# Performance work log

Hardware: AMD Instinct MI355X
Metric: run time of the kernel (lower is better)

Reference implementation:

```python
import jax, jax.numpy as jnp
import numpy as np

K = 2048          # codebook / vocab size (HMM N)
T = 1024          # time steps (HMM M)
NNZ = 4096        # sparse likelihood entries per mixture code (padded, static)
B = 16            # beam width
TEMPERATURE = 0.7


def setup_inputs() -> dict:
    key = jax.random.key(0)
    k0, k1, k2, k3, k4, k5 = jax.random.split(key, 6)
    prior0_table = jax.random.normal(k0, (K, K), dtype=jnp.float32)
    prior1_table = jax.random.normal(k1, (K, K), dtype=jnp.float32)
    # sparse log-likelihood values (log-domain, negative-ish)
    ll_data = jax.random.normal(k2, (T, NNZ), dtype=jnp.float32) - 2.0
    # coords: pairs (x0, x1) with nonzero likelihood for each mixture code
    ll_coords = jax.random.randint(k3, (T, 2, NNZ), 0, K, dtype=jnp.int32)
    x0_init = jax.random.randint(k4, (B,), 0, K, dtype=jnp.int32)  # SOS tokens
    x1_init = jax.random.randint(k5, (B,), 0, K, dtype=jnp.int32)
    return {"prior0_table": prior0_table, "prior1_table": prior1_table,
            "ll_data": ll_data, "ll_coords": ll_coords,
            "x0_init": x0_init, "x1_init": x1_init}


def _normalize_logits(logits, temperature):
    return jax.nn.log_softmax(logits / temperature, axis=-1)


def reference(prior0_table, prior1_table, ll_data, ll_coords, x0_init, x1_init):
    def step(carry, inputs):
        x0, x1, log_post_sum = carry            # [B], [B], [B]
        coords, data = inputs                   # [2, NNZ], [NNZ]
        log_p_0 = _normalize_logits(prior0_table[x0], TEMPERATURE)  # [B, K]
        log_p_1 = _normalize_logits(prior1_table[x1], TEMPERATURE)  # [B, K]
        # fused log posterior over sparse likelihood support: [B, NNZ]
        posterior = (log_post_sum[:, None] + data[None, :]
                     + log_p_0[:, coords[0]] + log_p_1[:, coords[1]])
        vals, idx = jax.lax.top_k(posterior.reshape(-1), B)  # prune to B beams
        coords_idx = idx % NNZ
        nx0 = coords[0, coords_idx]
        nx1 = coords[1, coords_idx]
        return (nx0, nx1, vals), (nx0, nx1)

    init = (x0_init, x1_init, jnp.zeros((B,), dtype=jnp.float32))
    (x0, x1, log_post_sum), (seq0, seq1) = jax.lax.scan(
        step, init, (ll_coords, ll_data))
    # final beam scores and decoded token sequences [T, B]
    return log_post_sum, seq0, seq1
```

## Files before the change

### kernel.cpp

```cpp
#include <hip/hip_runtime.h>
#include <hip/hip_bf16.h>
#include <math.h>
#include <stdint.h>

#define KDIM   2048
#define TSTEPS 1024
#define NNZ    4096
#define BEAMS  16
#define NWG    16
#define EPT    16
#define LCAP   4096

__device__ __forceinline__ float post_val(float lpsb, float d,
                                          float v0, float mm0, float ll0,
                                          float v1, float mm1, float ll1) {
    return ((lpsb + d) + ((v0 - mm0) - ll0)) + ((v1 - mm1) - ll1);
}

__device__ __forceinline__ uint32_t ord_enc(float f) {
    uint32_t u = __float_as_uint(f);
    return (u & 0x80000000u) ? ~u : (u | 0x80000000u);
}
__device__ __forceinline__ float ord_dec(uint32_t u) {
    return __uint_as_float((u & 0x80000000u) ? (u & 0x7FFFFFFFu) : ~u);
}

__global__ void scale_kernel(const float* __restrict__ p0,
                             const float* __restrict__ p1,
                             float* __restrict__ sc) {
    const int NF4 = (KDIM * KDIM) / 4;
    int i = blockIdx.x * blockDim.x + threadIdx.x;
    float4 v;
    if (i < NF4) v = ((const float4*)p0)[i];
    else         v = ((const float4*)p1)[i - NF4];
    v.x = v.x / 0.7f; v.y = v.y / 0.7f; v.z = v.z / 0.7f; v.w = v.w / 0.7f;
    ((float4*)sc)[i] = v;
}

__global__ void rowstat_kernel(const float* __restrict__ sc,
                               float* __restrict__ mArr,
                               float* __restrict__ lArr) {
    __shared__ float red[4];
    __shared__ float bm;
    const int r = blockIdx.x;
    const float* row = sc + (size_t)r * KDIM;
    const int tid = threadIdx.x;
    const int lane = tid & 63, wv = tid >> 6;

    float4 a = ((const float4*)row)[tid];
    float4 b = ((const float4*)row)[tid + 256];
    float m = fmaxf(fmaxf(fmaxf(a.x, a.y), fmaxf(a.z, a.w)),
                    fmaxf(fmaxf(b.x, b.y), fmaxf(b.z, b.w)));
    for (int s = 32; s; s >>= 1) m = fmaxf(m, __shfl_xor(m, s));
    if (lane == 0) red[wv] = m;
    __syncthreads();
    if (tid == 0) bm = fmaxf(fmaxf(red[0], red[1]), fmaxf(red[2], red[3]));
    __syncthreads();
    const float mm = bm;

    float s = expf(a.x - mm);
    s += expf(a.y - mm); s += expf(a.z - mm); s += expf(a.w - mm);
    s += expf(b.x - mm); s += expf(b.y - mm); s += expf(b.z - mm); s += expf(b.w - mm);
    for (int sh = 32; sh; sh >>= 1) s += __shfl_xor(s, sh);
    __syncthreads();
    if (lane == 0) red[wv] = s;
    __syncthreads();
    if (tid == 0) {
        float S = ((red[0] + red[1]) + red[2]) + red[3];
        mArr[r] = mm;
        lArr[r] = logf(S);
    }
}

__device__ __forceinline__ void bitonic64(float& v, int& i, int lane) {
    for (int k = 2; k <= 64; k <<= 1) {
        for (int j = k >> 1; j > 0; j >>= 1) {
            float ov = __shfl_xor(v, j);
            int   oi = __shfl_xor(i, j);
            bool lower = (lane & j) == 0;
            bool up    = (lane & k) == 0;
            bool iwin  = (v > ov) || (v == ov && i < oi);
            bool take  = (lower == up) ? !iwin : iwin;
            if (take) { v = ov; i = oi; }
        }
    }
}

__device__ __forceinline__ uint64_t bsort64(uint64_t v, int lane) {
    for (int k = 2; k <= 64; k <<= 1) {
        for (int j = k >> 1; j > 0; j >>= 1) {
            uint64_t ov = __shfl_xor((unsigned long long)v, j);
            bool lower = (lane & j) == 0;
            bool up    = (lane & k) == 0;
            bool iwin  = v > ov;
            bool take  = (lower == up) ? !iwin : iwin;
            if (take) v = ov;
        }
    }
    return v;
}

__device__ __forceinline__ float wave16th(float v, int lane) {
    int i = lane;
    bitonic64(v, i, lane);
    return __shfl(v, 15);
}

__device__ __forceinline__ void wave_top16(int C, float* cv, int* ci, int lane,
                                           float& myv, int& myi) {
    myv = -INFINITY; myi = 0x7FFFFFFF;
    if (C <= 64) {
        float v = (lane < C) ? cv[lane] : -INFINITY;
        int   i = (lane < C) ? ci[lane] : 0x7FFFFFFF;
        bitonic64(v, i, lane);
        myv = v; myi = i;
    } else {
        for (int rk = 0; rk < BEAMS; ++rk) {
            float bv = -INFINITY; int bi = 0x7FFFFFFF, bj = -1;
            for (int j = lane; j < C; j += 64) {
                float v = cv[j]; int ii = ci[j];
                if (v > bv || (v == bv && ii < bi)) { bv = v; bi = ii; bj = j; }
            }
            for (int s = 32; s; s >>= 1) {
                float ov = __shfl_xor(bv, s);
                int   oi = __shfl_xor(bi, s);
                int   oj = __shfl_xor(bj, s);
                if (ov > bv || (ov == bv && oi < bi)) { bv = ov; bi = oi; bj = oj; }
            }
            if (lane == rk) { myv = bv; myi = bi; }
            if (lane == 0) cv[bj] = -INFINITY;
        }
    }
}

__global__ __launch_bounds__(256, 1) void beam_kernel(
    const float* __restrict__ sc,
    const float* __restrict__ mArr,
    const float* __restrict__ lArr,
    const float* __restrict__ ll_data,
    const int*   __restrict__ ll_coords,
    const int*   __restrict__ x0i,
    const int*   __restrict__ x1i,
    float* __restrict__ out,
    uint64_t* __restrict__ gslot)
{
    __shared__ int   sx0[BEAMS], sx1[BEAMS];
    __shared__ float slps[BEAMS];
    __shared__ float wred[4];
    __shared__ int   scnt;
    __shared__ float cand_v[LCAP];
    __shared__ int   cand_i[LCAP];
    __shared__ uint64_t mg[64];
    __shared__ uint64_t respk[BEAMS];

    const int tid  = threadIdx.x;
    const int lane = tid & 63;
    const int wv   = tid >> 6;
    const int b    = blockIdx.x;
    const float* sc1 = sc + (size_t)KDIM * KDIM;
    const int n0 = tid * EPT;

    if (tid < BEAMS) { sx0[tid] = x0i[tid]; sx1[tid] = x1i[tid]; slps[tid] = 0.0f; }
    __syncthreads();

    float4 pf_d[4]; int4 pf_a[4], pf_b[4];
#pragma unroll
    for (int j = 0; j < 4; ++j) {
        pf_d[j] = *(const float4*)(ll_data + n0 + 4 * j);
        pf_a[j] = *(const int4*)(ll_coords + n0 + 4 * j);
        pf_b[j] = *(const int4*)(ll_coords + NNZ + n0 + 4 * j);
    }

#pragma unroll 1
    for (int t = 0; t < TSTEPS; ++t) {
        const int* cp = ll_coords + (size_t)t * 2 * NNZ;
        uint64_t* slots = gslot + (size_t)(t & 1) * (NWG * BEAMS);
        const uint32_t tag = (uint32_t)(t + 1);

        const int   r0i = sx0[b], r1i = sx1[b];
        const float* r0 = sc  + (size_t)r0i * KDIM;
        const float* r1 = sc1 + (size_t)r1i * KDIM;
        const float mm0 = mArr[r0i],        ll0 = lArr[r0i];
        const float mm1 = mArr[KDIM + r1i], ll1 = lArr[KDIM + r1i];
        const float lpsb = slps[b];

        if (tid == 0) scnt = 0;
        float p[EPT];
        float best = -INFINITY;
#pragma unroll
        for (int j = 0; j < 4; ++j) {
            float4 d4 = pf_d[j]; int4 a4 = pf_a[j]; int4 b4 = pf_b[j];
            float va0 = r0[a4.x], va1 = r0[a4.y], va2 = r0[a4.z], va3 = r0[a4.w];
            float vb0 = r1[b4.x], vb1 = r1[b4.y], vb2 = r1[b4.z], vb3 = r1[b4.w];
            p[4*j+0] = post_val(lpsb, d4.x, va0, mm0, ll0, vb0, mm1, ll1);
            p[4*j+1] = post_val(lpsb, d4.y, va1, mm0, ll0, vb1, mm1, ll1);
            p[4*j+2] = post_val(lpsb, d4.z, va2, mm0, ll0, vb2, mm1, ll1);
            p[4*j+3] = post_val(lpsb, d4.w, va3, mm0, ll0, vb3, mm1, ll1);
            best = fmaxf(best, fmaxf(fmaxf(p[4*j+0], p[4*j+1]), fmaxf(p[4*j+2], p[4*j+3])));
        }

        float w16 = wave16th(best, lane);
        if (lane == 0) wred[wv] = w16;
        __syncthreads();
        const float tau = fmaxf(fmaxf(wred[0], wred[1]), fmaxf(wred[2], wred[3]));

        if (best >= tau) {
#pragma unroll
            for (int j = 0; j < EPT; ++j) {
                if (p[j] >= tau) {
                    int pos = atomicAdd(&scnt, 1);
                    cand_v[pos] = p[j]; cand_i[pos] = (b << 12) | (n0 + j);
                }
            }
        }
        __syncthreads();

        {
            const int tp = (t + 1 < TSTEPS) ? t + 1 : t;
            const float* dp2 = ll_data + (size_t)tp * NNZ;
            const int*   cp2 = ll_coords + (size_t)tp * 2 * NNZ;
#pragma unroll
            for (int j = 0; j < 4; ++j) {
                pf_d[j] = *(const float4*)(dp2 + n0 + 4 * j);
                pf_a[j] = *(const int4*)(cp2 + n0 + 4 * j);
                pf_b[j] = *(const int4*)(cp2 + NNZ + n0 + 4 * j);
            }
        }

        if (wv == 0) {
            float myv; int myi;
            wave_top16(scnt, cand_v, cand_i, lane, myv, myi);
            if (lane < BEAMS) {
                uint64_t pk = ((uint64_t)ord_enc(myv) << 32)
                            | ((uint64_t)tag << 16)
                            | (uint64_t)((myi ^ 0xFFFF) & 0xFFFF);
                __hip_atomic_store(&slots[b * BEAMS + lane], pk,
                                   __ATOMIC_RELAXED, __HIP_MEMORY_SCOPE_AGENT);
            }
        }

        uint64_t pk;
        do {
            pk = __hip_atomic_load(&slots[tid], __ATOMIC_RELAXED,
                                   __HIP_MEMORY_SCOPE_AGENT);
        } while (((uint32_t)(pk >> 16) & 0xFFFFu) != tag);

        pk = bsort64(pk, lane);
        if (lane < BEAMS) mg[wv * BEAMS + lane] = pk;
        __syncthreads();
        if (wv == 0) {
            uint64_t q = bsort64(mg[lane], lane);
            if (lane < BEAMS) respk[lane] = q;
        }
        __syncthreads();

        if (tid < BEAMS) {
            uint64_t q = respk[tid];
            float v = ord_dec((uint32_t)(q >> 32));
            int idx = (int)((q & 0xFFFFu) ^ 0xFFFFu);
            int n = idx & (NNZ - 1);
            int tok0 = cp[n];
            int tok1 = cp[NNZ + n];
            sx0[tid] = tok0; sx1[tid] = tok1; slps[tid] = v;
            if (b == 0) {
                out[BEAMS + (size_t)t * BEAMS + tid] = (float)tok0;
                out[BEAMS + (size_t)TSTEPS * BEAMS + (size_t)t * BEAMS + tid] = (float)tok1;
                if (t == TSTEPS - 1) out[tid] = v;
            }
        }
        __syncthreads();
    }
}

extern "C" void kernel_launch(void* const* d_in, const int* in_sizes, int n_in,
                              void* d_out, int out_size, void* d_ws, size_t ws_size,
                              hipStream_t stream) {
    const float* p0        = (const float*)d_in[0];
    const float* p1        = (const float*)d_in[1];
    const float* ll_data   = (const float*)d_in[2];
    const int*   ll_coords = (const int*)d_in[3];
    const int*   x0i       = (const int*)d_in[4];
    const int*   x1i       = (const int*)d_in[5];
    float* outp = (float*)d_out;

    float* sc   = (float*)d_ws;
    float* mArr = sc + (size_t)2 * KDIM * KDIM;
    float* lArr = mArr + 2 * KDIM;
    uint64_t* gslot = (uint64_t*)(lArr + 2 * KDIM);

    scale_kernel<<<(2 * KDIM * KDIM / 4) / 256, 256, 0, stream>>>(p0, p1, sc);
    rowstat_kernel<<<2 * KDIM, 256, 0, stream>>>(sc, mArr, lArr);
    beam_kernel<<<NWG, 256, 0, stream>>>(sc, mArr, lArr, ll_data, ll_coords,
                                         x0i, x1i, outp, gslot);
}
```

Baseline: 17.71 ms.

## Pack candidates as u64 keys, ballot-compact them, and threshold-prune the cross-workgroup merge

Candidates are now stored as packed 64-bit (ordered value, index) keys, so selection compares one integer instead of value plus index. They are appended to LDS through wave ballot plus mbcnt, which replaces one LDS atomic per element with one per wave. The global merge takes the minimum of each workgroup's head key as a threshold and keeps only keys at or above it before a single wave selects the top 16. That replaces the two-level bitonic merge and lets every thread read its next beam state from registers. Spin polling now sleeps between tries, and the linear top-16 fallback on large candidate sets may cost more per step.

```diff
diff --git a/kernel.cpp b/kernel.cpp
--- a/kernel.cpp
+++ b/kernel.cpp
@@ -23,6 +23,11 @@
 }
 __device__ __forceinline__ float ord_dec(uint32_t u) {
     return __uint_as_float((u & 0x80000000u) ? (u & 0x7FFFFFFFu) : ~u);
+}
+
+__device__ __forceinline__ int lane_offset(uint64_t mask) {
+    return __builtin_amdgcn_mbcnt_hi((uint32_t)(mask >> 32),
+           __builtin_amdgcn_mbcnt_lo((uint32_t)mask, 0u));
 }
 
 __global__ void scale_kernel(const float* __restrict__ p0,
@@ -72,18 +77,18 @@
     }
 }
 
-__device__ __forceinline__ void bitonic64(float& v, int& i, int lane) {
+__device__ __forceinline__ float wave16th_f(float v, int lane) {
     for (int k = 2; k <= 64; k <<= 1) {
         for (int j = k >> 1; j > 0; j >>= 1) {
             float ov = __shfl_xor(v, j);
-            int   oi = __shfl_xor(i, j);
             bool lower = (lane & j) == 0;
             bool up    = (lane & k) == 0;
-            bool iwin  = (v > ov) || (v == ov && i < oi);
+            bool iwin  = v > ov;
             bool take  = (lower == up) ? !iwin : iwin;
-            if (take) { v = ov; i = oi; }
-        }
-    }
+            if (take) v = ov;
+        }
+    }
+    return __shfl(v, 15);
 }
 
 __device__ __forceinline__ uint64_t bsort64(uint64_t v, int lane) {
@@ -100,37 +105,27 @@
     return v;
 }
 
-__device__ __forceinline__ float wave16th(float v, int lane) {
-    int i = lane;
-    bitonic64(v, i, lane);
-    return __shfl(v, 15);
-}
-
-__device__ __forceinline__ void wave_top16(int C, float* cv, int* ci, int lane,
-                                           float& myv, int& myi) {
-    myv = -INFINITY; myi = 0x7FFFFFFF;
+__device__ __forceinline__ uint64_t wave_sel16_u64(int C, uint64_t* lds, int lane) {
     if (C <= 64) {
-        float v = (lane < C) ? cv[lane] : -INFINITY;
-        int   i = (lane < C) ? ci[lane] : 0x7FFFFFFF;
-        bitonic64(v, i, lane);
-        myv = v; myi = i;
-    } else {
-        for (int rk = 0; rk < BEAMS; ++rk) {
-            float bv = -INFINITY; int bi = 0x7FFFFFFF, bj = -1;
-            for (int j = lane; j < C; j += 64) {
-                float v = cv[j]; int ii = ci[j];
-                if (v > bv || (v == bv && ii < bi)) { bv = v; bi = ii; bj = j; }
-            }
-            for (int s = 32; s; s >>= 1) {
-                float ov = __shfl_xor(bv, s);
-                int   oi = __shfl_xor(bi, s);
-                int   oj = __shfl_xor(bj, s);
-                if (ov > bv || (ov == bv && oi < bi)) { bv = ov; bi = oi; bj = oj; }
-            }
-            if (lane == rk) { myv = bv; myi = bi; }
-            if (lane == 0) cv[bj] = -INFINITY;
-        }
-    }
+        uint64_t v = (lane < C) ? lds[lane] : 0;
+        return bsort64(v, lane);
+    }
+    uint64_t res = 0;
+    for (int rk = 0; rk < BEAMS; ++rk) {
+        uint64_t bv = 0; int bj = -1;
+        for (int j = lane; j < C; j += 64) {
+            uint64_t v = lds[j];
+            if (v > bv) { bv = v; bj = j; }
+        }
+        for (int s = 32; s; s >>= 1) {
+            uint64_t ov = __shfl_xor((unsigned long long)bv, s);
+            int      oj = __shfl_xor(bj, s);
+            if (ov > bv) { bv = ov; bj = oj; }
+        }
+        if (lane == 0 && bj >= 0) lds[bj] = 0;
+        if (lane == rk) res = bv;
+    }
+    return res;
 }
 
 __global__ __launch_bounds__(256, 1) void beam_kernel(
@@ -144,13 +139,10 @@
     float* __restrict__ out,
     uint64_t* __restrict__ gslot)
 {
-    __shared__ int   sx0[BEAMS], sx1[BEAMS];
-    __shared__ float slps[BEAMS];
-    __shared__ float wred[4];
-    __shared__ int   scnt;
-    __shared__ float cand_v[LCAP];
-    __shared__ int   cand_i[LCAP];
-    __shared__ uint64_t mg[64];
+    __shared__ float    wred[4];
+    __shared__ int      scnt;
+    __shared__ uint64_t cand_pk[LCAP];
+    __shared__ uint64_t headq[NWG];
     __shared__ uint64_t respk[BEAMS];
 
     const int tid  = threadIdx.x;
@@ -160,8 +152,9 @@
     const float* sc1 = sc + (size_t)KDIM * KDIM;
     const int n0 = tid * EPT;
 
-    if (tid < BEAMS) { sx0[tid] = x0i[tid]; sx1[tid] = x1i[tid]; slps[tid] = 0.0f; }
-    __syncthreads();
+    int   r0i  = x0i[b];
+    int   r1i  = x1i[b];
+    float lpsb = 0.0f;
 
     float4 pf_d[4]; int4 pf_a[4], pf_b[4];
 #pragma unroll
@@ -177,14 +170,13 @@
         uint64_t* slots = gslot + (size_t)(t & 1) * (NWG * BEAMS);
         const uint32_t tag = (uint32_t)(t + 1);
 
-        const int   r0i = sx0[b], r1i = sx1[b];
+        if (tid == 0) scnt = 0;
+
         const float* r0 = sc  + (size_t)r0i * KDIM;
         const float* r1 = sc1 + (size_t)r1i * KDIM;
         const float mm0 = mArr[r0i],        ll0 = lArr[r0i];
         const float mm1 = mArr[KDIM + r1i], ll1 = lArr[KDIM + r1i];
-        const float lpsb = slps[b];
-
-        if (tid == 0) scnt = 0;
+
         float p[EPT];
         float best = -INFINITY;
 #pragma unroll
@@ -199,21 +191,10 @@
             best = fmaxf(best, fmaxf(fmaxf(p[4*j+0], p[4*j+1]), fmaxf(p[4*j+2], p[4*j+3])));
         }
 
-        float w16 = wave16th(best, lane);
+        float w16 = wave16th_f(best, lane);
         if (lane == 0) wred[wv] = w16;
         __syncthreads();
         const float tau = fmaxf(fmaxf(wred[0], wred[1]), fmaxf(wred[2], wred[3]));
-
-        if (best >= tau) {
-#pragma unroll
-            for (int j = 0; j < EPT; ++j) {
-                if (p[j] >= tau) {
-                    int pos = atomicAdd(&scnt, 1);
-                    cand_v[pos] = p[j]; cand_i[pos] = (b << 12) | (n0 + j);
-                }
-            }
-        }
-        __syncthreads();
 
         {
             const int tp = (t + 1 < TSTEPS) ? t + 1 : t;
@@ -227,14 +208,28 @@
             }
         }
 
+#pragma unroll 1
+        for (int j = 0; j < EPT; ++j) {
+            bool q = (p[j] >= tau);
+            uint64_t mask = __ballot(q);
+            if (mask) {
+                int base;
+                if (lane == 0) base = atomicAdd(&scnt, __builtin_popcountll(mask));
+                base = __shfl(base, 0);
+                if (q) {
+                    uint32_t idx16 = (uint32_t)((b << 12) | (n0 + j));
+                    cand_pk[base + lane_offset(mask)] =
+                        ((uint64_t)ord_enc(p[j]) << 32) | (uint64_t)((idx16 ^ 0xFFFFu) & 0xFFFFu);
+                }
+            }
+        }
+        __syncthreads();
+
         if (wv == 0) {
-            float myv; int myi;
-            wave_top16(scnt, cand_v, cand_i, lane, myv, myi);
+            uint64_t q = wave_sel16_u64(scnt, cand_pk, lane);
             if (lane < BEAMS) {
-                uint64_t pk = ((uint64_t)ord_enc(myv) << 32)
-                            | ((uint64_t)tag << 16)
-                            | (uint64_t)((myi ^ 0xFFFF) & 0xFFFF);
-                __hip_atomic_store(&slots[b * BEAMS + lane], pk,
+                __hip_atomic_store(&slots[b * BEAMS + lane],
+                                   q | ((uint64_t)tag << 16),
                                    __ATOMIC_RELAXED, __HIP_MEMORY_SCOPE_AGENT);
             }
         }
@@ -243,30 +238,48 @@
         do {
             pk = __hip_atomic_load(&slots[tid], __ATOMIC_RELAXED,
                                    __HIP_MEMORY_SCOPE_AGENT);
-        } while (((uint32_t)(pk >> 16) & 0xFFFFu) != tag);
-
-        pk = bsort64(pk, lane);
-        if (lane < BEAMS) mg[wv * BEAMS + lane] = pk;
-        __syncthreads();
+            if (((uint32_t)(pk >> 16) & 0xFFFFu) == tag) break;
+            __builtin_amdgcn_s_sleep(1);
+        } while (true);
+
+        if ((tid & 15) == 0) headq[tid >> 4] = pk;
+        if (tid == 0) scnt = 0;
+        __syncthreads();
+
+        uint64_t tq = headq[0];
+#pragma unroll
+        for (int k = 1; k < NWG; ++k) tq = (headq[k] < tq) ? headq[k] : tq;
+        {
+            bool qq = (pk >= tq);
+            uint64_t mask = __ballot(qq);
+            int base;
+            if (lane == 0) base = atomicAdd(&scnt, __builtin_popcountll(mask));
+            base = __shfl(base, 0);
+            if (qq) cand_pk[base + lane_offset(mask)] = pk;
+        }
+        __syncthreads();
+
         if (wv == 0) {
-            uint64_t q = bsort64(mg[lane], lane);
+            uint64_t q = wave_sel16_u64(scnt, cand_pk, lane);
             if (lane < BEAMS) respk[lane] = q;
         }
         __syncthreads();
 
-        if (tid < BEAMS) {
+        {
+            uint64_t qb = respk[b];
+            int idx = (int)((qb & 0xFFFFu) ^ 0xFFFFu);
+            int n = idx & (NNZ - 1);
+            r0i = cp[n];
+            r1i = cp[NNZ + n];
+            lpsb = ord_dec((uint32_t)(qb >> 32));
+        }
+        if (b == 0 && tid < BEAMS) {
             uint64_t q = respk[tid];
-            float v = ord_dec((uint32_t)(q >> 32));
             int idx = (int)((q & 0xFFFFu) ^ 0xFFFFu);
             int n = idx & (NNZ - 1);
-            int tok0 = cp[n];
-            int tok1 = cp[NNZ + n];
-            sx0[tid] = tok0; sx1[tid] = tok1; slps[tid] = v;
-            if (b == 0) {
-                out[BEAMS + (size_t)t * BEAMS + tid] = (float)tok0;
-                out[BEAMS + (size_t)TSTEPS * BEAMS + (size_t)t * BEAMS + tid] = (float)tok1;
-                if (t == TSTEPS - 1) out[tid] = v;
-            }
+            out[BEAMS + (size_t)t * BEAMS + tid] = (float)cp[n];
+            out[BEAMS + (size_t)TSTEPS * BEAMS + (size_t)t * BEAMS + tid] = (float)cp[NNZ + n];
+            if (t == TSTEPS - 1) out[tid] = ord_dec((uint32_t)(q >> 32));
         }
         __syncthreads();
     }
```

New measurement: 18.38 ms. 1.04x slower.
